# Kernel optimization log

Measured on AMD Instinct MI355X. Metric: run time of the kernel, lower is better.

The kernel has to match this reference:

```python
import jax, jax.numpy as jnp
import numpy as np

CUTOFF_RATIO = 4
FS = 8000.0
ZEROS = 8
HALF = int(ZEROS * CUTOFF_RATIO / 2)          # 16
FILTER_SIZE = 2 * HALF + 1                     # 33


def _sinc(x):
    # sin(x)/x with safe gradient at 0 (input NOT multiplied by pi)
    xs = jnp.where(x == 0, 1.0, x)
    return jnp.where(x == 0, 1.0, jnp.sin(xs) / xs)


def _filters(n, alpha, beta):
    # per-timestep cutoff: (pi/r + alpha*sin(beta*t/fs)) / (2*pi)   -> (n,)
    t = jnp.arange(n, dtype=jnp.float32)
    cutoff = (jnp.pi / CUTOFF_RATIO + alpha * jnp.sin(beta * t / FS)) / (2.0 * jnp.pi)
    # hann window, periodic=False, length FILTER_SIZE
    k = jnp.arange(FILTER_SIZE, dtype=jnp.float32)
    window = 0.5 - 0.5 * jnp.cos(2.0 * jnp.pi * k / (FILTER_SIZE - 1))
    time = jnp.arange(-HALF, HALF + 1, dtype=jnp.float32)
    f = 2.0 * cutoff[:, None] * window[None, :] * _sinc(2.0 * jnp.pi * cutoff[:, None] * time[None, :])
    f = f / f.sum(axis=-1, keepdims=True)      # (n, FILTER_SIZE)
    return f[:, ::-1]                           # flipped, as in compute_conv_mat


def setup_inputs() -> dict:
    key = jax.random.key(0)
    k1, k2, k3 = jax.random.split(key, 3)
    x = jax.random.normal(k1, (64, 32768), dtype=jnp.float32)
    alpha = jax.random.uniform(k2, (), dtype=jnp.float32) * 0.5   # keep cutoff_t > 0
    beta = jax.random.uniform(k3, (), dtype=jnp.float32) * 4.0
    return {"input": x, "alpha": alpha, "beta": beta}


def reference(input, alpha, beta):
    # Time-varying FIR: identical math to building the (n, n) banded conv_mat
    # (rows t cover original cols t..t+filter_size-1, then sliced to cols
    # half_size..n+half_size-1) followed by matmul -- without the n^2 matrix.
    n = input.shape[-1]
    filt = _filters(n, alpha, beta)                              # (n, K)
    xpad = jnp.pad(input, ((0, 0), (HALF, HALF)))                # (B, n+2*HALF)
    idx = jnp.arange(n)[:, None] + jnp.arange(FILTER_SIZE)[None, :]  # (n, K)
    windows = xpad[:, idx]                                       # (B, n, K)
    return jnp.einsum('tk,btk->bt', filt, windows)
```

## Files before the change

### kernel.cpp

```cpp
#include <hip/hip_runtime.h>
#include <math.h>


constexpr int   HALF   = 16;
constexpr int   FSZ    = 33;
constexpr float PI_F   = 3.14159265358979323846f;
constexpr int   BLOCK  = 256;
constexpr int   ROWS_PER_BLOCK = 8;

template <bool CHECK>
__device__ __forceinline__ void lpf_body(const float* __restrict__ x,
                                         float* __restrict__ out,
                                         float alpha, float beta,
                                         int n, int t, int row0)
{
    const float cutoff = (PI_F / 4.0f + alpha * sinf(beta * (float)t / 8000.0f))
                         / (2.0f * PI_F);

    float c[FSZ];
    float sum = 0.0f;
    #pragma unroll
    for (int j = 1; j < FSZ - 1; ++j) {
        const float w   = 0.5f - 0.5f * cosf((2.0f * PI_F / (float)(FSZ - 1)) * (float)j);
        const float tm  = (float)(j - HALF);
        float s;
        if (j == HALF) {
            s = 1.0f;
        } else {
            const float arg = 2.0f * PI_F * cutoff * tm;
            s = sinf(arg) / arg;
        }
        const float f = 2.0f * cutoff * w * s;
        c[j] = f;
        sum += f;
    }
    const float inv = 1.0f / sum;
    #pragma unroll
    for (int j = 1; j < FSZ - 1; ++j) c[j] *= inv;

    for (int r = 0; r < ROWS_PER_BLOCK; ++r) {
        const float* __restrict__ base = x + (size_t)(row0 + r) * (size_t)n;
        float acc = 0.0f;
        #pragma unroll
        for (int j = 1; j < FSZ - 1; ++j) {
            const int idx = t + HALF - j;
            float v;
            if (CHECK) {
                v = (idx >= 0 && idx < n) ? base[idx] : 0.0f;
            } else {
                v = base[idx];
            }
            acc = fmaf(c[j], v, acc);
        }
        out[(size_t)(row0 + r) * (size_t)n + t] = acc;
    }
}

__global__ __launch_bounds__(BLOCK)
void LowPassFilter_53661321396356_kernel(const float* __restrict__ x,
                                         const float* __restrict__ alpha_p,
                                         const float* __restrict__ beta_p,
                                         float* __restrict__ out,
                                         int n)
{
    const int t = blockIdx.x * BLOCK + threadIdx.x;
    if (t >= n) return;
    const int row0  = blockIdx.y * ROWS_PER_BLOCK;
    const float alpha = alpha_p[0];
    const float beta  = beta_p[0];

    if (blockIdx.x == 0 || blockIdx.x == gridDim.x - 1) {
        lpf_body<true >(x, out, alpha, beta, n, t, row0);
    } else {
        lpf_body<false>(x, out, alpha, beta, n, t, row0);
    }
}

extern "C" void kernel_launch(void* const* d_in, const int* in_sizes, int n_in,
                              void* d_out, int out_size, void* d_ws, size_t ws_size,
                              hipStream_t stream) {
    const float* x       = (const float*)d_in[0];
    const float* alpha_p = (const float*)d_in[1];
    const float* beta_p  = (const float*)d_in[2];
    float*       out     = (float*)d_out;

    const int B = 64;
    const int n = in_sizes[0] / B;

    dim3 grid((n + BLOCK - 1) / BLOCK, B / ROWS_PER_BLOCK);
    dim3 block(BLOCK);
    LowPassFilter_53661321396356_kernel<<<grid, block, 0, stream>>>(
        x, alpha_p, beta_p, out, n);
}
```

Measured before the change: 26.38 us.

## Compute filter taps via Chebyshev sine recurrence and vectorize four outputs per thread

Replaces the per-tap sinf/cosf filter construction with a single sincos plus a Chebyshev recurrence for sin(k*theta), taking the Hann window and 1/(pi*k) factors from a constexpr table. It also exploits tap symmetry to halve the multiplies. Each thread now produces four adjacent outputs, using float4 loads of a shared 36-sample window and float4 stores, and rows per block drop from 8 to 4. The aim is to remove transcendental-heavy coefficient math and cut load instructions. The risks are small numerical drift from the recurrence, and register pressure from the 4x16 coefficient array plus the 36-element window.

```diff
diff --git a/kernel.cpp b/kernel.cpp
--- a/kernel.cpp
+++ b/kernel.cpp
@@ -2,57 +2,95 @@
 #include <math.h>
 
 
-constexpr int   HALF   = 16;
-constexpr int   FSZ    = 33;
-constexpr float PI_F   = 3.14159265358979323846f;
-constexpr int   BLOCK  = 256;
-constexpr int   ROWS_PER_BLOCK = 8;
+constexpr int   HALF  = 16;
+constexpr int   BLOCK = 256;
+constexpr int   VEC   = 4;
+constexpr int   ROWS  = 4;
+constexpr float PI_F  = 3.14159265358979323846f;
+constexpr double PI_D = 3.14159265358979323846;
+
+constexpr float W_TAB[16] = {
+    0.0f,
+    (float)((0.5 + 0.5 *  0.98078528040323044) / (PI_D *  1.0)),
+    (float)((0.5 + 0.5 *  0.92387953251128674) / (PI_D *  2.0)),
+    (float)((0.5 + 0.5 *  0.83146961230254524) / (PI_D *  3.0)),
+    (float)((0.5 + 0.5 *  0.70710678118654752) / (PI_D *  4.0)),
+    (float)((0.5 + 0.5 *  0.55557023301960222) / (PI_D *  5.0)),
+    (float)((0.5 + 0.5 *  0.38268343236508977) / (PI_D *  6.0)),
+    (float)((0.5 + 0.5 *  0.19509032201612827) / (PI_D *  7.0)),
+    (float)((0.5 + 0.5 *  0.0                ) / (PI_D *  8.0)),
+    (float)((0.5 + 0.5 * -0.19509032201612827) / (PI_D *  9.0)),
+    (float)((0.5 + 0.5 * -0.38268343236508977) / (PI_D * 10.0)),
+    (float)((0.5 + 0.5 * -0.55557023301960222) / (PI_D * 11.0)),
+    (float)((0.5 + 0.5 * -0.70710678118654752) / (PI_D * 12.0)),
+    (float)((0.5 + 0.5 * -0.83146961230254524) / (PI_D * 13.0)),
+    (float)((0.5 + 0.5 * -0.92387953251128674) / (PI_D * 14.0)),
+    (float)((0.5 + 0.5 * -0.98078528040323044) / (PI_D * 15.0)),
+};
 
 template <bool CHECK>
 __device__ __forceinline__ void lpf_body(const float* __restrict__ x,
                                          float* __restrict__ out,
                                          float alpha, float beta,
-                                         int n, int t, int row0)
+                                         int n, int t0, int row0)
 {
-    const float cutoff = (PI_F / 4.0f + alpha * sinf(beta * (float)t / 8000.0f))
-                         / (2.0f * PI_F);
+    float C[VEC][16];
+    #pragma unroll
+    for (int o = 0; o < VEC; ++o) {
+        const float tf    = (float)(t0 + o);
+        const float theta = 0.25f * PI_F + alpha * sinf(beta * tf * (1.0f / 8000.0f));
+        float s1, c1;
+        sincosf(theta, &s1, &c1);
 
-    float c[FSZ];
-    float sum = 0.0f;
-    #pragma unroll
-    for (int j = 1; j < FSZ - 1; ++j) {
-        const float w   = 0.5f - 0.5f * cosf((2.0f * PI_F / (float)(FSZ - 1)) * (float)j);
-        const float tm  = (float)(j - HALF);
-        float s;
-        if (j == HALF) {
-            s = 1.0f;
+        float f[16];
+        f[0] = theta * (float)(1.0 / PI_D);
+        f[1] = s1 * W_TAB[1];
+        const float two_c = 2.0f * c1;
+        float skm1 = s1, skm2 = 0.0f;
+        #pragma unroll
+        for (int k = 2; k < 16; ++k) {
+            const float sk = fmaf(two_c, skm1, -skm2);
+            f[k] = sk * W_TAB[k];
+            skm2 = skm1; skm1 = sk;
+        }
+        float sum = f[0];
+        #pragma unroll
+        for (int k = 1; k < 16; ++k) sum += 2.0f * f[k];
+        const float inv = 1.0f / sum;
+        #pragma unroll
+        for (int k = 0; k < 16; ++k) C[o][k] = f[k] * inv;
+    }
+
+    for (int r = 0; r < ROWS; ++r) {
+        const float* __restrict__ base = x + (size_t)(row0 + r) * (size_t)n;
+        float w[36];
+        if (CHECK) {
+            #pragma unroll
+            for (int i = 0; i < 36; ++i) {
+                const int idx = t0 - 16 + i;
+                w[i] = (idx >= 0 && idx < n) ? base[idx] : 0.0f;
+            }
         } else {
-            const float arg = 2.0f * PI_F * cutoff * tm;
-            s = sinf(arg) / arg;
+            const float4* __restrict__ p = (const float4*)(base + t0 - 16);
+            #pragma unroll
+            for (int q = 0; q < 9; ++q) {
+                const float4 v = p[q];
+                w[4*q+0] = v.x; w[4*q+1] = v.y; w[4*q+2] = v.z; w[4*q+3] = v.w;
+            }
         }
-        const float f = 2.0f * cutoff * w * s;
-        c[j] = f;
-        sum += f;
-    }
-    const float inv = 1.0f / sum;
-    #pragma unroll
-    for (int j = 1; j < FSZ - 1; ++j) c[j] *= inv;
 
-    for (int r = 0; r < ROWS_PER_BLOCK; ++r) {
-        const float* __restrict__ base = x + (size_t)(row0 + r) * (size_t)n;
-        float acc = 0.0f;
+        float4 res;
+        float* rp = &res.x;
         #pragma unroll
-        for (int j = 1; j < FSZ - 1; ++j) {
-            const int idx = t + HALF - j;
-            float v;
-            if (CHECK) {
-                v = (idx >= 0 && idx < n) ? base[idx] : 0.0f;
-            } else {
-                v = base[idx];
-            }
-            acc = fmaf(c[j], v, acc);
+        for (int o = 0; o < VEC; ++o) {
+            const int ci = o + 16;
+            float acc = C[o][0] * w[ci];
+            #pragma unroll
+            for (int k = 1; k < 16; ++k)
+                acc = fmaf(C[o][k], w[ci - k] + w[ci + k], acc);
+            rp[o] = acc;
         }
-        out[(size_t)(row0 + r) * (size_t)n + t] = acc;
+        *(float4*)(out + (size_t)(row0 + r) * (size_t)n + t0) = res;
     }
 }
 
@@ -63,16 +101,16 @@
                                          float* __restrict__ out,
                                          int n)
 {
-    const int t = blockIdx.x * BLOCK + threadIdx.x;
-    if (t >= n) return;
-    const int row0  = blockIdx.y * ROWS_PER_BLOCK;
+    const int t0 = (blockIdx.x * BLOCK + threadIdx.x) * VEC;
+    if (t0 >= n) return;
+    const int row0   = blockIdx.y * ROWS;
     const float alpha = alpha_p[0];
     const float beta  = beta_p[0];
 
     if (blockIdx.x == 0 || blockIdx.x == gridDim.x - 1) {
-        lpf_body<true >(x, out, alpha, beta, n, t, row0);
+        lpf_body<true >(x, out, alpha, beta, n, t0, row0);
     } else {
-        lpf_body<false>(x, out, alpha, beta, n, t, row0);
+        lpf_body<false>(x, out, alpha, beta, n, t0, row0);
     }
 }
 
@@ -87,7 +125,7 @@
     const int B = 64;
     const int n = in_sizes[0] / B;
 
-    dim3 grid((n + BLOCK - 1) / BLOCK, B / ROWS_PER_BLOCK);
+    dim3 grid((n + BLOCK * VEC - 1) / (BLOCK * VEC), B / ROWS);
     dim3 block(BLOCK);
     LowPassFilter_53661321396356_kernel<<<grid, block, 0, stream>>>(
         x, alpha_p, beta_p, out, n);
```

Result: faster. 23.88 us (-9.5%).
